# Performance work log

Hardware: AMD Instinct MI355X
Metric: run time of the kernel (lower is better)

Reference implementation:

```python
import jax, jax.numpy as jnp
import numpy as np

D_MODEL = 1024
N_HEADS = 16
HEAD_DIM = D_MODEL // N_HEADS
D_FF = 4 * D_MODEL
EPS = 1e-5


def _layer_norm(h, g, b):
    m = jnp.mean(h, axis=-1, keepdims=True)
    v = jnp.mean(jnp.square(h - m), axis=-1, keepdims=True)
    return (h - m) * jax.lax.rsqrt(v + EPS) * g + b


def setup_inputs() -> dict:
    key = jax.random.key(0)
    ks = jax.random.split(key, 10)
    B, S, D = 4, 2048, D_MODEL
    scale = 0.02
    inp = {
        "x": jax.random.normal(ks[0], (B, S, D), dtype=jnp.float32),
        "Wq": scale * jax.random.normal(ks[1], (D, D), dtype=jnp.float32),
        "Wk": scale * jax.random.normal(ks[2], (D, D), dtype=jnp.float32),
        "Wv": scale * jax.random.normal(ks[3], (D, D), dtype=jnp.float32),
        "Wo": scale * jax.random.normal(ks[4], (D, D), dtype=jnp.float32),
        "ln1_g": jnp.ones((D,), dtype=jnp.float32),
        "ln1_b": jnp.zeros((D,), dtype=jnp.float32),
        "ln2_g": jnp.ones((D,), dtype=jnp.float32),
        "ln2_b": jnp.zeros((D,), dtype=jnp.float32),
        "W1": scale * jax.random.normal(ks[5], (D, D_FF), dtype=jnp.float32),
        "b1": jnp.zeros((D_FF,), dtype=jnp.float32),
        "W2": scale * jax.random.normal(ks[6], (D_FF, D), dtype=jnp.float32),
        "b2": jnp.zeros((D,), dtype=jnp.float32),
        "Wc": scale * jax.random.normal(ks[7], (D, 1), dtype=jnp.float32),
        "bc": jnp.zeros((1,), dtype=jnp.float32),
    }
    return inp


def reference(x, Wq, Wk, Wv, Wo, ln1_g, ln1_b, ln2_g, ln2_b, W1, b1, W2, b2, Wc, bc):
    B, S, D = x.shape
    H, hd = N_HEADS, HEAD_DIM
    # --- causal self-attention (pre-LN) ---
    h = _layer_norm(x, ln1_g, ln1_b)
    q = (h @ Wq).reshape(B, S, H, hd).transpose(0, 2, 1, 3)  # [B,H,S,hd]
    k = (h @ Wk).reshape(B, S, H, hd).transpose(0, 2, 1, 3)
    v = (h @ Wv).reshape(B, S, H, hd).transpose(0, 2, 1, 3)
    scores = jnp.einsum("bhqd,bhkd->bhqk", q, k) / jnp.sqrt(jnp.asarray(hd, x.dtype))
    causal = jnp.triu(jnp.ones((S, S), dtype=bool), k=1)
    scores = jnp.where(causal[None, None, :, :], -jnp.inf, scores)
    attn = jax.nn.softmax(scores, axis=-1)
    ctx = jnp.einsum("bhqk,bhkd->bhqd", attn, v).transpose(0, 2, 1, 3).reshape(B, S, D)
    x1 = x + ctx @ Wo
    # --- FFN (pre-LN, ReLU) ---
    h2 = _layer_norm(x1, ln2_g, ln2_b)
    ff = jax.nn.relu(h2 @ W1 + b1) @ W2 + b2
    x_out = x1 + ff
    # --- adaptive confidence gate: mean-pool seq -> Linear -> sigmoid -> batch mean ---
    pooled = jnp.mean(x_out, axis=1)  # [B,D]
    conf = jnp.mean(jax.nn.sigmoid(pooled @ Wc + bc), axis=0)  # [1]
    return x_out, conf
```

## Files before the change

### kernel.cpp

```cpp
#include <hip/hip_runtime.h>
#include <hip/hip_bf16.h>

typedef __hip_bfloat16 bf16;
typedef __attribute__((ext_vector_type(8))) short short8;
typedef __attribute__((ext_vector_type(4))) float f32x4;

#define D_MODELC 1024
#define D_FFC    4096
#define NHEADS   16
#define HDIM     64
#define SEQLEN   2048
#define BATCHN   4
#define MTOT     (BATCHN * SEQLEN)

__device__ __forceinline__ void async16(void* lds, const void* g) {
  __builtin_amdgcn_global_load_lds(
      (const __attribute__((address_space(1))) unsigned int*)g,
      (__attribute__((address_space(3))) unsigned int*)lds, 16, 0, 0);
}

__global__ __launch_bounds__(256) void transpose_bf16_k(
    const float* __restrict__ src, bf16* __restrict__ dst, int R, int C, float scale) {
  __shared__ float tile[32][33];
  int tx = threadIdx.x & 31, ty = threadIdx.x >> 5;
  int r0 = blockIdx.y * 32, c0 = blockIdx.x * 32;
#pragma unroll
  for (int i = 0; i < 4; i++) {
    int r = ty + i * 8;
    tile[r][tx] = src[(size_t)(r0 + r) * C + c0 + tx];
  }
  __syncthreads();
#pragma unroll
  for (int i = 0; i < 4; i++) {
    int c = ty + i * 8;
    dst[(size_t)(c0 + c) * R + r0 + tx] = __float2bfloat16(tile[tx][c] * scale);
  }
}

__global__ __launch_bounds__(256) void ln_bf16_k(
    const float* __restrict__ x, const float* __restrict__ g,
    const float* __restrict__ b, bf16* __restrict__ out) {
  int row = blockIdx.x;
  int t = threadIdx.x;
  f32x4 v = ((const f32x4*)(x + (size_t)row * D_MODELC))[t];
  float s = v[0] + v[1] + v[2] + v[3];
  float ss = v[0] * v[0] + v[1] * v[1] + v[2] * v[2] + v[3] * v[3];
#pragma unroll
  for (int m = 1; m < 64; m <<= 1) {
    s += __shfl_xor(s, m);
    ss += __shfl_xor(ss, m);
  }
  __shared__ float red[8];
  int w = t >> 6, l = t & 63;
  if (l == 0) { red[w] = s; red[4 + w] = ss; }
  __syncthreads();
  s = red[0] + red[1] + red[2] + red[3];
  ss = red[4] + red[5] + red[6] + red[7];
  float mean = s * (1.0f / D_MODELC);
  float var = ss * (1.0f / D_MODELC) - mean * mean;
  float rs = rsqrtf(var + 1e-5f);
  f32x4 gv = ((const f32x4*)g)[t];
  f32x4 bv = ((const f32x4*)b)[t];
  unsigned short u[4];
#pragma unroll
  for (int j = 0; j < 4; j++) {
    float o = (v[j] - mean) * rs * gv[j] + bv[j];
    u[j] = __bfloat16_as_ushort(__float2bfloat16(o));
  }
  unsigned int lo = (unsigned int)u[0] | ((unsigned int)u[1] << 16);
  unsigned int hi = (unsigned int)u[2] | ((unsigned int)u[3] << 16);
  ((uint2*)(out + (size_t)row * D_MODELC))[t] = make_uint2(lo, hi);
}

#define BM 128
#define BN 128
#define BKK 32

enum { EPI_QKV = 0, EPI_RESID = 1, EPI_BIAS_RELU = 2, EPI_BIAS_RESID = 3 };

template <int EPI>
__global__ __launch_bounds__(256) void gemm_nt(
    const bf16* __restrict__ A, const bf16* __restrict__ BT, int M, int N, int K,
    const float* __restrict__ bias, const float* __restrict__ resid,
    float* __restrict__ outF, bf16* __restrict__ outB) {
  __shared__ bf16 As[BM * BKK];
  __shared__ bf16 Bs[BN * BKK];
  const int t = threadIdx.x;
  const int l = t & 63;
  const int w = t >> 6;
  const int wm = w >> 1, wn = w & 1;

  int nwg = gridDim.x * gridDim.y;
  int bid = blockIdx.y * gridDim.x + blockIdx.x;
  if ((nwg & 7) == 0) {
    int q8 = nwg >> 3;
    bid = (bid & 7) * q8 + (bid >> 3);
  }
  const int bx = bid % gridDim.x, by = bid / gridDim.x;
  const int m0 = by * BM, n0 = bx * BN;
  const int lr = l & 15, lk = (l >> 4) * 8;

  f32x4 acc[4][4];
#pragma unroll
  for (int i = 0; i < 4; i++)
#pragma unroll
    for (int j = 0; j < 4; j++) acc[i][j] = (f32x4){0.f, 0.f, 0.f, 0.f};

  const char* Abase = (const char*)(A + (size_t)m0 * K);
  const char* Bbase = (const char*)(BT + (size_t)n0 * K);

  for (int k0 = 0; k0 < K; k0 += BKK) {
#pragma unroll
    for (int c = 0; c < 2; c++) {
      int off = (c * 256 + t) * 16;
      int r = off >> 6;
      int cb = off & 63;
      async16((char*)As + off, Abase + ((size_t)r * K + k0) * 2 + cb);
      async16((char*)Bs + off, Bbase + ((size_t)r * K + k0) * 2 + cb);
    }
    __syncthreads();
    short8 a[4], b[4];
#pragma unroll
    for (int mi = 0; mi < 4; mi++)
      a[mi] = *(const short8*)&As[(wm * 64 + mi * 16 + lr) * BKK + lk];
#pragma unroll
    for (int ni = 0; ni < 4; ni++)
      b[ni] = *(const short8*)&Bs[(wn * 64 + ni * 16 + lr) * BKK + lk];
#pragma unroll
    for (int mi = 0; mi < 4; mi++)
#pragma unroll
      for (int ni = 0; ni < 4; ni++)
        acc[mi][ni] = __builtin_amdgcn_mfma_f32_16x16x32_bf16(a[mi], b[ni], acc[mi][ni], 0, 0, 0);
    __syncthreads();
  }

#pragma unroll
  for (int mi = 0; mi < 4; mi++) {
#pragma unroll
    for (int ni = 0; ni < 4; ni++) {
#pragma unroll
      for (int j = 0; j < 4; j++) {
        int gm = m0 + wm * 64 + mi * 16 + ((l >> 4) * 4) + j;
        int gn = n0 + wn * 64 + ni * 16 + lr;
        float v = acc[mi][ni][j];
        if constexpr (EPI == EPI_QKV) {
          int sel = gn >> 10, d = gn & 1023;
          int b_ = gm >> 11, s_ = gm & 2047;
          int h2 = d >> 6, dd = d & 63;
          size_t bh = (size_t)b_ * NHEADS + h2;
          size_t dst;
          if (sel < 2) {
            dst = (size_t)sel * ((size_t)MTOT * D_MODELC) +
                  (bh * SEQLEN + s_) * HDIM + dd;
          } else {
            dst = 2 * ((size_t)MTOT * D_MODELC) +
                  (bh * HDIM + dd) * SEQLEN + s_;
          }
          outB[dst] = __float2bfloat16(v);
        } else if constexpr (EPI == EPI_RESID) {
          size_t idx = (size_t)gm * N + gn;
          outF[idx] = resid[idx] + v;
        } else if constexpr (EPI == EPI_BIAS_RELU) {
          float z = v + bias[gn];
          outB[(size_t)gm * N + gn] = __float2bfloat16(z > 0.f ? z : 0.f);
        } else {
          size_t idx = (size_t)gm * N + gn;
          outF[idx] = resid[idx] + v + bias[gn];
        }
      }
    }
  }
}

#define KVB 64
#define PSTR 76

__global__ __launch_bounds__(256) void attn_k(
    const bf16* __restrict__ qg, const bf16* __restrict__ kg,
    const bf16* __restrict__ vtg, bf16* __restrict__ ctx) {
  const int bid = blockIdx.x;
  const int qt = (SEQLEN / KVB - 1) - (bid >> 6);
  const int bh = bid & 63;
  const int q0 = qt * 64;
  const int t = threadIdx.x, w = t >> 6, l = t & 63;
  const int lr = l & 15, lkg = l >> 4, lk = lkg * 8;

  const bf16* Q  = qg  + (size_t)bh * SEQLEN * HDIM;
  const bf16* Kg = kg  + (size_t)bh * SEQLEN * HDIM;
  const bf16* Vt = vtg + (size_t)bh * HDIM * SEQLEN;

  __shared__ bf16 Ks[KVB * PSTR];
  __shared__ bf16 Vs[HDIM * PSTR];
  __shared__ bf16 Ps[4][16 * PSTR];

  short8 qf[2];
  const int qrow = q0 + w * 16 + lr;
#pragma unroll
  for (int kk = 0; kk < 2; kk++)
    qf[kk] = *(const short8*)&Q[(size_t)qrow * HDIM + kk * 32 + lk];

  const short8 bones = {0x3F80, 0x3F80, 0x3F80, 0x3F80, 0x3F80, 0x3F80, 0x3F80, 0x3F80};

  f32x4 o[4];
  f32x4 ol = (f32x4){0.f, 0.f, 0.f, 0.f};
#pragma unroll
  for (int nh = 0; nh < 4; nh++) o[nh] = (f32x4){0.f, 0.f, 0.f, 0.f};

  const int srow = t >> 3;
  const int scc  = (t & 7) * 8;

  const int ntiles = qt + 1;
  for (int tkv = 0; tkv < ntiles; tkv++) {
    const int kv0 = tkv * KVB;
#pragma unroll
    for (int r = 0; r < 2; r++) {
      int row = srow + r * 32;
      short8 kv = *(const short8*)&Kg[(size_t)(kv0 + row) * HDIM + scc];
      *(short8*)&Ks[row * PSTR + scc] = kv;
      short8 vv = *(const short8*)&Vt[(size_t)row * SEQLEN + kv0 + scc];
      *(short8*)&Vs[row * PSTR + scc] = vv;
    }
    __syncthreads();

    short8 kf[4][2];
#pragma unroll
    for (int ni = 0; ni < 4; ni++)
#pragma unroll
      for (int kk = 0; kk < 2; kk++)
        kf[ni][kk] = *(const short8*)&Ks[(ni * 16 + lr) * PSTR + kk * 32 + lk];
    f32x4 s[4];
#pragma unroll
    for (int ni = 0; ni < 4; ni++) {
      f32x4 a = (f32x4){0.f, 0.f, 0.f, 0.f};
#pragma unroll
      for (int kk = 0; kk < 2; kk++)
        a = __builtin_amdgcn_mfma_f32_16x16x32_bf16(qf[kk], kf[ni][kk], a, 0, 0, 0);
      s[ni] = a;
    }
    if (tkv == ntiles - 1) {
#pragma unroll
      for (int ni = 0; ni < 4; ni++)
#pragma unroll
        for (int j = 0; j < 4; j++) {
          int qq = q0 + w * 16 + lkg * 4 + j;
          int kv = kv0 + ni * 16 + lr;
          if (kv > qq) s[ni][j] = -1e30f;
        }
    }
#pragma unroll
    for (int ni = 0; ni < 4; ni++)
#pragma unroll
      for (int j = 0; j < 4; j++)
        ((short*)Ps[w])[(lkg * 4 + j) * PSTR + ni * 16 + lr] =
            (short)__bfloat16_as_ushort(__float2bfloat16(exp2f(s[ni][j])));
#pragma unroll
    for (int kk = 0; kk < 2; kk++) {
      short8 pa = *(const short8*)&Ps[w][lr * PSTR + kk * 32 + lk];
      ol = __builtin_amdgcn_mfma_f32_16x16x32_bf16(pa, bones, ol, 0, 0, 0);
#pragma unroll
      for (int nh = 0; nh < 4; nh++) {
        short8 vb = *(const short8*)&Vs[(nh * 16 + lr) * PSTR + kk * 32 + lk];
        o[nh] = __builtin_amdgcn_mfma_f32_16x16x32_bf16(pa, vb, o[nh], 0, 0, 0);
      }
    }
    __syncthreads();
  }

  const int b_ = bh >> 4, h_ = bh & 15;
#pragma unroll
  for (int j = 0; j < 4; j++) {
    float inv = 1.0f / ol[j];
    int qq = q0 + w * 16 + lkg * 4 + j;
    size_t base = (((size_t)b_ * SEQLEN + qq) * NHEADS + h_) * HDIM;
#pragma unroll
    for (int nh = 0; nh < 4; nh++)
      ctx[base + nh * 16 + lr] = __float2bfloat16(o[nh][j] * inv);
  }
}

__global__ __launch_bounds__(256) void pool_partial_k(
    const float* __restrict__ xo, float* __restrict__ part) {
  int blk = blockIdx.x;
  int b_ = blk >> 4, ch = blk & 15;
  int t = threadIdx.x;
  f32x4 acc = (f32x4){0.f, 0.f, 0.f, 0.f};
  const float* base = xo + ((size_t)b_ * SEQLEN + (size_t)ch * 128) * D_MODELC;
  for (int r = 0; r < 128; r++)
    acc += ((const f32x4*)(base + (size_t)r * D_MODELC))[t];
  ((f32x4*)(part + (size_t)blk * D_MODELC))[t] = acc;
}

__global__ __launch_bounds__(256) void conf_k(
    const float* __restrict__ part, const float* __restrict__ Wc,
    const float* __restrict__ bc, float* __restrict__ outc) {
  int t = threadIdx.x;
  __shared__ float red[4];
  float total = 0.f;
  for (int b_ = 0; b_ < BATCHN; b_++) {
    f32x4 sum = (f32x4){0.f, 0.f, 0.f, 0.f};
    for (int ch = 0; ch < 16; ch++)
      sum += ((const f32x4*)(part + (size_t)(b_ * 16 + ch) * D_MODELC))[t];
    f32x4 wv = ((const f32x4*)Wc)[t];
    float d = (sum[0] * wv[0] + sum[1] * wv[1] + sum[2] * wv[2] + sum[3] * wv[3]) * (1.0f / SEQLEN);
#pragma unroll
    for (int m = 1; m < 64; m <<= 1) d += __shfl_xor(d, m);
    int wq = t >> 6, l = t & 63;
    if (l == 0) red[wq] = d;
    __syncthreads();
    float z = red[0] + red[1] + red[2] + red[3] + bc[0];
    total += 1.0f / (1.0f + __expf(-z));
    __syncthreads();
  }
  if (t == 0) outc[0] = total * (1.0f / BATCHN);
}

extern "C" void kernel_launch(void* const* d_in, const int* in_sizes, int n_in,
                              void* d_out, int out_size, void* d_ws, size_t ws_size,
                              hipStream_t stream) {
  const float* x    = (const float*)d_in[0];
  const float* Wq   = (const float*)d_in[1];
  const float* Wk   = (const float*)d_in[2];
  const float* Wv   = (const float*)d_in[3];
  const float* Wo   = (const float*)d_in[4];
  const float* ln1g = (const float*)d_in[5];
  const float* ln1b = (const float*)d_in[6];
  const float* ln2g = (const float*)d_in[7];
  const float* ln2b = (const float*)d_in[8];
  const float* W1   = (const float*)d_in[9];
  const float* b1   = (const float*)d_in[10];
  const float* W2   = (const float*)d_in[11];
  const float* b2   = (const float*)d_in[12];
  const float* Wc   = (const float*)d_in[13];
  const float* bc   = (const float*)d_in[14];

  char* ws = (char*)d_ws;
  const size_t MB = 1024 * 1024;
  bf16* qkv   = (bf16*)(ws);
  bf16* ctx   = (bf16*)(ws + 48 * MB);
  bf16* ff1   = (bf16*)(ws);
  bf16* h     = (bf16*)(ws + 64 * MB);
  bf16* WqkvT = (bf16*)(ws + 80 * MB);
  bf16* WoT   = (bf16*)(ws + 86 * MB);
  bf16* W1T   = (bf16*)(ws + 88 * MB);
  bf16* W2T   = (bf16*)(ws + 96 * MB);
  float* part = (float*)(ws + 104 * MB);

  float* xout = (float*)d_out;
  dim3 blk(256);

  const float SCL2 = 0.125f * 1.44269504f;

  transpose_bf16_k<<<dim3(32, 32), blk, 0, stream>>>(Wq, WqkvT, 1024, 1024, SCL2);
  transpose_bf16_k<<<dim3(32, 32), blk, 0, stream>>>(Wk, WqkvT + 1024 * 1024, 1024, 1024, 1.0f);
  transpose_bf16_k<<<dim3(32, 32), blk, 0, stream>>>(Wv, WqkvT + 2 * 1024 * 1024, 1024, 1024, 1.0f);
  transpose_bf16_k<<<dim3(32, 32), blk, 0, stream>>>(Wo, WoT, 1024, 1024, 1.0f);
  transpose_bf16_k<<<dim3(128, 32), blk, 0, stream>>>(W1, W1T, 1024, 4096, 1.0f);
  transpose_bf16_k<<<dim3(32, 128), blk, 0, stream>>>(W2, W2T, 4096, 1024, 1.0f);

  ln_bf16_k<<<MTOT, blk, 0, stream>>>(x, ln1g, ln1b, h);
  gemm_nt<EPI_QKV><<<dim3(3072 / BN, MTOT / BM), blk, 0, stream>>>(
      h, WqkvT, MTOT, 3072, 1024, nullptr, nullptr, nullptr, qkv);
  attn_k<<<dim3((SEQLEN / KVB) * 64), blk, 0, stream>>>(
      qkv, qkv + (size_t)MTOT * D_MODELC, qkv + 2 * (size_t)MTOT * D_MODELC, ctx);
  gemm_nt<EPI_RESID><<<dim3(1024 / BN, MTOT / BM), blk, 0, stream>>>(
      ctx, WoT, MTOT, 1024, 1024, nullptr, x, xout, nullptr);
  ln_bf16_k<<<MTOT, blk, 0, stream>>>(xout, ln2g, ln2b, h);
  gemm_nt<EPI_BIAS_RELU><<<dim3(4096 / BN, MTOT / BM), blk, 0, stream>>>(
      h, W1T, MTOT, 4096, 1024, b1, nullptr, nullptr, ff1);
  gemm_nt<EPI_BIAS_RESID><<<dim3(1024 / BN, MTOT / BM), blk, 0, stream>>>(
      ff1, W2T, MTOT, 1024, 4096, b2, xout, xout, nullptr);
  pool_partial_k<<<64, blk, 0, stream>>>(xout, part);
  conf_k<<<1, blk, 0, stream>>>(part, Wc, bc, xout + (size_t)MTOT * D_MODELC);
}
```

Baseline: 474.3 us.

## Double GEMM K-tile to 64 with XOR-swizzled LDS layout

Raises the GEMM K-step from 32 to 64, so each main-loop iteration loads twice as much A/B data and issues twice as many MFMAs per pair of barriers. The LDS tiles are stored with an XOR swizzle of the 16-byte segment index against the row, applied when loading from global and when reading from LDS, to avoid bank conflicts on the wider 128-byte rows. The cost is double the LDS per block (32KB) and more fragment registers, which may reduce occupancy.

```diff
diff --git a/kernel.cpp b/kernel.cpp
--- a/kernel.cpp
+++ b/kernel.cpp
@@ -74,7 +74,7 @@
 
 #define BM 128
 #define BN 128
-#define BKK 32
+#define BKK 64
 
 enum { EPI_QKV = 0, EPI_RESID = 1, EPI_BIAS_RELU = 2, EPI_BIAS_RESID = 3 };
 
@@ -98,7 +98,7 @@
   }
   const int bx = bid % gridDim.x, by = bid / gridDim.x;
   const int m0 = by * BM, n0 = bx * BN;
-  const int lr = l & 15, lk = (l >> 4) * 8;
+  const int lr = l & 15, lkg = l >> 4;
 
   f32x4 acc[4][4];
 #pragma unroll
@@ -111,26 +111,37 @@
 
   for (int k0 = 0; k0 < K; k0 += BKK) {
 #pragma unroll
-    for (int c = 0; c < 2; c++) {
+    for (int c = 0; c < 4; c++) {
       int off = (c * 256 + t) * 16;
-      int r = off >> 6;
-      int cb = off & 63;
-      async16((char*)As + off, Abase + ((size_t)r * K + k0) * 2 + cb);
-      async16((char*)Bs + off, Bbase + ((size_t)r * K + k0) * 2 + cb);
-    }
-    __syncthreads();
-    short8 a[4], b[4];
-#pragma unroll
-    for (int mi = 0; mi < 4; mi++)
-      a[mi] = *(const short8*)&As[(wm * 64 + mi * 16 + lr) * BKK + lk];
-#pragma unroll
-    for (int ni = 0; ni < 4; ni++)
-      b[ni] = *(const short8*)&Bs[(wn * 64 + ni * 16 + lr) * BKK + lk];
-#pragma unroll
-    for (int mi = 0; mi < 4; mi++)
-#pragma unroll
-      for (int ni = 0; ni < 4; ni++)
-        acc[mi][ni] = __builtin_amdgcn_mfma_f32_16x16x32_bf16(a[mi], b[ni], acc[mi][ni], 0, 0, 0);
+      int r = off >> 7;
+      int sg = ((off >> 4) & 7) ^ (r & 7);
+      async16((char*)As + off, Abase + ((size_t)r * K + k0) * 2 + sg * 16);
+      async16((char*)Bs + off, Bbase + ((size_t)r * K + k0) * 2 + sg * 16);
+    }
+    __syncthreads();
+    short8 a[2][4], b[2][4];
+#pragma unroll
+    for (int kk = 0; kk < 2; kk++) {
+#pragma unroll
+      for (int mi = 0; mi < 4; mi++) {
+        int row = wm * 64 + mi * 16 + lr;
+        int sl = (kk * 4 + lkg) ^ (row & 7);
+        a[kk][mi] = *(const short8*)((const char*)As + row * 128 + sl * 16);
+      }
+#pragma unroll
+      for (int ni = 0; ni < 4; ni++) {
+        int row = wn * 64 + ni * 16 + lr;
+        int sl = (kk * 4 + lkg) ^ (row & 7);
+        b[kk][ni] = *(const short8*)((const char*)Bs + row * 128 + sl * 16);
+      }
+    }
+#pragma unroll
+    for (int kk = 0; kk < 2; kk++)
+#pragma unroll
+      for (int mi = 0; mi < 4; mi++)
+#pragma unroll
+        for (int ni = 0; ni < 4; ni++)
+          acc[mi][ni] = __builtin_amdgcn_mfma_f32_16x16x32_bf16(a[kk][mi], b[kk][ni], acc[mi][ni], 0, 0, 0);
     __syncthreads();
   }
 
```

Measured after the change: 427.5 us. 9.9% less time.
